# Performance work log

Measured on AMD Instinct MI355X. Metric: run time of the kernel, lower is better.

## Reference

```python
import jax, jax.numpy as jnp
import numpy as np

N, D, H, E_RAW = 100000, 128, 8, 1600000
C = D // H  # head dim = 16
NEG_SLOPE = 0.2
LN_EPS = 1e-5


def _glorot(key, shape):
    fan_in, fan_out = shape[0], shape[-1]
    lim = (6.0 / (fan_in + fan_out)) ** 0.5
    return jax.random.uniform(key, shape, jnp.float32, -lim, lim)


def setup_inputs() -> dict:
    key = jax.random.key(0)
    ks = jax.random.split(key, 16)
    inp = {
        "x": jax.random.normal(ks[0], (N, D), jnp.float32),
        "edge_index": jax.random.randint(ks[1], (2, E_RAW), 0, N, jnp.int64),
    }
    for l in range(2):
        o = 2 + 4 * l
        inp[f"Wl{l}"] = _glorot(ks[o + 0], (D, H * C))
        inp[f"Wr{l}"] = _glorot(ks[o + 1], (D, H * C))
        inp[f"att{l}"] = _glorot(ks[o + 2], (H, C))
        inp[f"b{l}"] = jnp.zeros((H * C,), jnp.float32)
        inp[f"g{l}"] = jnp.ones((D,), jnp.float32)
        inp[f"beta{l}"] = jnp.zeros((D,), jnp.float32)
    return inp


def _gatv2_layer(x, src, dst, Wl, Wr, att, b):
    # GATv2Conv: e_ij = att . leaky_relu(Wl x_j + Wr x_i); softmax over j -> i
    xl = (x @ Wl).reshape(N, H, C)  # source transform
    xr = (x @ Wr).reshape(N, H, C)  # target transform
    m = jax.nn.leaky_relu(xl[src] + xr[dst], NEG_SLOPE)  # [E,H,C]
    e = jnp.einsum("ehc,hc->eh", m, att)  # [E,H]
    emax = jax.ops.segment_max(e, dst, num_segments=N)[dst]
    ex = jnp.exp(e - emax)
    denom = jax.ops.segment_sum(ex, dst, num_segments=N)[dst]
    alpha = ex / denom  # per-destination softmax
    out = jax.ops.segment_sum(xl[src] * alpha[:, :, None], dst, num_segments=N)
    return out.reshape(N, H * C) + b


def _layernorm(x, g, beta):
    mu = jnp.mean(x, axis=-1, keepdims=True)
    var = jnp.var(x, axis=-1, keepdims=True)
    return (x - mu) * jax.lax.rsqrt(var + LN_EPS) * g + beta


def reference(x, edge_index, Wl0, Wr0, att0, b0, g0, beta0,
              Wl1, Wr1, att1, b1, g1, beta1):
    # add_self_loops=True (PyG default): every node attends to itself
    loop = jnp.arange(N, dtype=edge_index.dtype)
    src = jnp.concatenate([edge_index[0], loop])
    dst = jnp.concatenate([edge_index[1], loop])
    params = [(Wl0, Wr0, att0, b0, g0, beta0), (Wl1, Wr1, att1, b1, g1, beta1)]
    for Wl, Wr, att, b, g, beta in params:
        residual = x
        h = _gatv2_layer(x, src, dst, Wl, Wr, att, b)  # dropout is identity (eval)
        h = jax.nn.elu(h)
        x = _layernorm(h + residual, g, beta)
    return x
```

## Files before the change

kernel.cpp:

```cpp
#include <hip/hip_runtime.h>
#include <cstdint>

#define LEAKY 0.2f
#define LN_EPS 1e-5f

typedef __attribute__((ext_vector_type(8))) short short8;
typedef __attribute__((ext_vector_type(4))) float f32x4;
typedef __attribute__((ext_vector_type(2))) float f32x2;

__device__ __forceinline__ ushort bf16_rne(float x) {
    unsigned u = __float_as_uint(x);
    unsigned r = (u + 0x7fffu + ((u >> 16) & 1u)) >> 16;
    return (ushort)r;
}
__device__ __forceinline__ float bf16_to_f(ushort h) {
    return __uint_as_float(((unsigned)h) << 16);
}

__global__ void hist_part(const int* __restrict__ ei, int er, int etot, int n,
                          int* __restrict__ deg) {
    const int xcd = blockIdx.x & 7;
    const int lo = (int)((long long)n * xcd >> 3);
    const int hi = (int)((long long)n * (xcd + 1) >> 3);
    const int stride = (gridDim.x >> 3) * blockDim.x;
    for (int e = (blockIdx.x >> 3) * blockDim.x + threadIdx.x; e < etot;
         e += stride) {
        int dst = (e < er) ? ei[er + e] : (e - er);
        if (dst >= lo && dst < hi) atomicAdd(&deg[dst], 1);
    }
}

__global__ void fill_part(const int* __restrict__ ei, int er, int etot, int n,
                          int* __restrict__ woff, int* __restrict__ colv) {
    const int xcd = blockIdx.x & 7;
    const int lo = (int)((long long)n * xcd >> 3);
    const int hi = (int)((long long)n * (xcd + 1) >> 3);
    const int stride = (gridDim.x >> 3) * blockDim.x;
    for (int e = (blockIdx.x >> 3) * blockDim.x + threadIdx.x; e < etot;
         e += stride) {
        int dst = (e < er) ? ei[er + e] : (e - er);
        if (dst >= lo && dst < hi) {
            int src = (e < er) ? ei[e] : dst;
            int pos = atomicAdd(&woff[dst], 1);
            colv[pos] = src;
        }
    }
}

__global__ __launch_bounds__(1024) void scanA(const int* __restrict__ deg,
                                              int* __restrict__ escan,
                                              int* __restrict__ bsum, int n) {
    __shared__ int wsum[16], wpre[16];
    const int lane = threadIdx.x & 63, wv = threadIdx.x >> 6;
    const int i = blockIdx.x * 1024 + threadIdx.x;
    int v = (i < n) ? deg[i] : 0;
    int x = v;
#pragma unroll
    for (int off = 1; off < 64; off <<= 1) {
        int y = __shfl_up(x, off, 64);
        if (lane >= off) x += y;
    }
    if (lane == 63) wsum[wv] = x;
    __syncthreads();
    if (wv == 0) {
        int s = (lane < 16) ? wsum[lane] : 0;
#pragma unroll
        for (int off = 1; off < 16; off <<= 1) {
            int y = __shfl_up(s, off, 64);
            if (lane >= off) s += y;
        }
        if (lane < 16) wpre[lane] = s;
    }
    __syncthreads();
    int excl = x - v + (wv ? wpre[wv - 1] : 0);
    if (i < n) escan[i] = excl;
    if (threadIdx.x == 1023) bsum[blockIdx.x] = wpre[15];
}

__global__ __launch_bounds__(1024) void scanB(const int* __restrict__ bsum,
                                              int* __restrict__ bpre, int nb,
                                              int* __restrict__ offs, int n) {
    __shared__ int wsum[16], wpre[16];
    const int lane = threadIdx.x & 63, wv = threadIdx.x >> 6;
    const int i = threadIdx.x;
    int v = (i < nb) ? bsum[i] : 0;
    int x = v;
#pragma unroll
    for (int off = 1; off < 64; off <<= 1) {
        int y = __shfl_up(x, off, 64);
        if (lane >= off) x += y;
    }
    if (lane == 63) wsum[wv] = x;
    __syncthreads();
    if (wv == 0) {
        int s = (lane < 16) ? wsum[lane] : 0;
#pragma unroll
        for (int off = 1; off < 16; off <<= 1) {
            int y = __shfl_up(s, off, 64);
            if (lane >= off) s += y;
        }
        if (lane < 16) wpre[lane] = s;
    }
    __syncthreads();
    if (i < nb) bpre[i] = x - v + (wv ? wpre[wv - 1] : 0);
    if (threadIdx.x == 1023) offs[n] = wpre[15];
}

__global__ void scanC(const int* __restrict__ escan, const int* __restrict__ bpre,
                      int* __restrict__ offs, int* __restrict__ woff, int n) {
    int i = blockIdx.x * 256 + threadIdx.x;
    if (i >= n) return;
    int o = escan[i] + bpre[i >> 10];
    offs[i] = o;
    woff[i] = o;
}

__global__ void cvt_w2(const float* __restrict__ Wl0, const float* __restrict__ Wr0,
                       const float* __restrict__ Wl1, const float* __restrict__ Wr1,
                       ushort* __restrict__ Whi, ushort* __restrict__ Wlo) {
    int t = blockIdx.x * 256 + threadIdx.x;
    int layer = t >> 15;
    int i = t & 32767;
    int colblk = i >> 11;
    int ks = (i >> 9) & 3;
    int lane = (i >> 3) & 63;
    int j = i & 7;
    int col = colblk * 16 + (lane & 15);
    int k = ks * 32 + (lane >> 4) * 8 + j;
    const float* Wl = layer ? Wl1 : Wl0;
    const float* Wr = layer ? Wr1 : Wr0;
    float v = (col < 128) ? Wl[(size_t)k * 128 + col]
                          : Wr[(size_t)k * 128 + (col - 128)];
    ushort h = bf16_rne(v);
    Whi[t] = h;
    Wlo[t] = bf16_rne(v - bf16_to_f(h));
}

__global__ __launch_bounds__(256) void gemm_mfma(
    const float* __restrict__ X,
    const ushort* __restrict__ Wfhi, const ushort* __restrict__ Wflo,
    uint* __restrict__ Olb, uint* __restrict__ Orb, int nrows) {
    __shared__ float xs[64 * 32 * 4];
    const int t = threadIdx.x;
    const int wave = t >> 6, lane = t & 63;
    const int m0 = blockIdx.x * 64;
    {
        const float4* Xv = (const float4*)X + (size_t)m0 * 32;
        float4* xsv = (float4*)xs;
#pragma unroll
        for (int i = 0; i < 8; ++i) {
            int idx = i * 256 + t;
            int row = idx >> 5, kc = idx & 31;
            float4 v = {0.f, 0.f, 0.f, 0.f};
            if (m0 + row < nrows) v = Xv[idx];
            xsv[row * 32 + (kc ^ (row & 7))] = v;
        }
    }
    __syncthreads();

    const int lrow = lane & 15;
    const int lkc = (lane >> 4) * 2;
    f32x4 acc[4][4];
#pragma unroll
    for (int mt = 0; mt < 4; ++mt)
#pragma unroll
        for (int nt = 0; nt < 4; ++nt) acc[mt][nt] = (f32x4){0.f, 0.f, 0.f, 0.f};

#pragma unroll 1
    for (int ks = 0; ks < 4; ++ks) {
        short8 ahi[4], alo[4];
#pragma unroll
        for (int mt = 0; mt < 4; ++mt) {
            const int row = mt * 16 + lrow;
            const int kc0 = ks * 8 + lkc;
            float4 v0 = ((const float4*)xs)[row * 32 + (kc0 ^ (row & 7))];
            float4 v1 = ((const float4*)xs)[row * 32 + ((kc0 + 1) ^ (row & 7))];
            float e[8];
            e[0] = v0.x; e[1] = v0.y; e[2] = v0.z; e[3] = v0.w;
            e[4] = v1.x; e[5] = v1.y; e[6] = v1.z; e[7] = v1.w;
#pragma unroll
            for (int j = 0; j < 8; ++j) {
                ushort h = (ushort)(__float_as_uint(e[j]) >> 16);
                ahi[mt][j] = (short)h;
                alo[mt][j] = (short)bf16_rne(e[j] - bf16_to_f(h));
            }
        }
#pragma unroll
        for (int nt = 0; nt < 4; ++nt) {
            size_t off = (((size_t)(wave * 4 + nt) * 4 + ks) * 64 + lane) * 8;
            short8 bhi = *(const short8*)&Wfhi[off];
            short8 blo = *(const short8*)&Wflo[off];
#pragma unroll
            for (int mt = 0; mt < 4; ++mt) {
                acc[mt][nt] = __builtin_amdgcn_mfma_f32_16x16x32_bf16(
                    alo[mt], bhi, acc[mt][nt], 0, 0, 0);
                acc[mt][nt] = __builtin_amdgcn_mfma_f32_16x16x32_bf16(
                    ahi[mt], blo, acc[mt][nt], 0, 0, 0);
                acc[mt][nt] = __builtin_amdgcn_mfma_f32_16x16x32_bf16(
                    ahi[mt], bhi, acc[mt][nt], 0, 0, 0);
            }
        }
    }
    uint* __restrict__ O = (wave < 2) ? Olb : Orb;
    const int cbase = (wave * 64) & 127;
    const int crow0 = (lane >> 4) * 4;
    const bool evn = (lane & 1) == 0;
#pragma unroll
    for (int mt = 0; mt < 4; ++mt) {
#pragma unroll
        for (int i = 0; i < 4; ++i) {
            const int row = m0 + mt * 16 + crow0 + i;
#pragma unroll
            for (int nt = 0; nt < 4; ++nt) {
                float val = acc[mt][nt][i];
                float pv = __shfl_xor(val, 1);
                uint pk = (uint)bf16_rne(val) | ((uint)bf16_rne(pv) << 16);
                if (evn && row < nrows) {
                    const int col = cbase + nt * 16 + lrow;
                    O[(size_t)row * 64 + (col >> 1)] = pk;
                }
            }
        }
    }
}

__global__ __launch_bounds__(256) void gat_agg(
    const uint* __restrict__ xl, const uint* __restrict__ xr,
    const int* __restrict__ offs, const int* __restrict__ colv,
    const float* __restrict__ att,
    const float* __restrict__ bias, const float* __restrict__ gamma,
    const float* __restrict__ beta, const float* __restrict__ resid,
    float* __restrict__ out, int nnode) {
    const int lane = threadIdx.x & 63;
    const int wave0 = blockIdx.x * 4 + (threadIdx.x >> 6);
    const int wstride = gridDim.x * 4;
    const uint* __restrict__ xlb = xl + lane;
    const f32x2 att2 = ((const f32x2*)att)[lane];
    const f32x2 b2 = ((const f32x2*)bias)[lane];
    const f32x2 g2 = ((const f32x2*)gamma)[lane];
    const f32x2 be2 = ((const f32x2*)beta)[lane];
    for (int gid = wave0; gid < nnode; gid += wstride) {
        const uint xru = __builtin_nontemporal_load(xr + (size_t)gid * 64 + lane);
        const float xrx = __uint_as_float(xru << 16);
        const float xry = __uint_as_float(xru & 0xffff0000u);
        float den = 0.f, acc0 = 0.f, acc1 = 0.f;
        int e = offs[gid];
        const int e1 = offs[gid + 1];
        for (; e + 4 <= e1; e += 4) {
            int s0 = colv[e], s1 = colv[e + 1], s2 = colv[e + 2], s3 = colv[e + 3];
            uint u0 = xlb[(size_t)s0 * 64];
            uint u1 = xlb[(size_t)s1 * 64];
            uint u2 = xlb[(size_t)s2 * 64];
            uint u3 = xlb[(size_t)s3 * 64];
            float a0x = __uint_as_float(u0 << 16), a0y = __uint_as_float(u0 & 0xffff0000u);
            float a1x = __uint_as_float(u1 << 16), a1y = __uint_as_float(u1 & 0xffff0000u);
            float a2x = __uint_as_float(u2 << 16), a2y = __uint_as_float(u2 & 0xffff0000u);
            float a3x = __uint_as_float(u3 << 16), a3y = __uint_as_float(u3 & 0xffff0000u);
            float m0x = a0x + xrx, m0y = a0y + xry;
            float m1x = a1x + xrx, m1y = a1y + xry;
            float m2x = a2x + xrx, m2y = a2y + xry;
            float m3x = a3x + xrx, m3y = a3y + xry;
            m0x = fmaxf(m0x, LEAKY * m0x); m0y = fmaxf(m0y, LEAKY * m0y);
            m1x = fmaxf(m1x, LEAKY * m1x); m1y = fmaxf(m1y, LEAKY * m1y);
            m2x = fmaxf(m2x, LEAKY * m2x); m2y = fmaxf(m2y, LEAKY * m2y);
            m3x = fmaxf(m3x, LEAKY * m3x); m3y = fmaxf(m3y, LEAKY * m3y);
            float p0 = m0x * att2.x + m0y * att2.y;
            float p1 = m1x * att2.x + m1y * att2.y;
            float p2 = m2x * att2.x + m2y * att2.y;
            float p3 = m3x * att2.x + m3y * att2.y;
            p0 += __shfl_xor(p0, 1); p0 += __shfl_xor(p0, 2); p0 += __shfl_xor(p0, 4);
            p1 += __shfl_xor(p1, 1); p1 += __shfl_xor(p1, 2); p1 += __shfl_xor(p1, 4);
            p2 += __shfl_xor(p2, 1); p2 += __shfl_xor(p2, 2); p2 += __shfl_xor(p2, 4);
            p3 += __shfl_xor(p3, 1); p3 += __shfl_xor(p3, 2); p3 += __shfl_xor(p3, 4);
            float ex0 = __expf(p0), ex1 = __expf(p1);
            float ex2 = __expf(p2), ex3 = __expf(p3);
            den += (ex0 + ex1) + (ex2 + ex3);
            acc0 += a0x * ex0 + a1x * ex1 + a2x * ex2 + a3x * ex3;
            acc1 += a0y * ex0 + a1y * ex1 + a2y * ex2 + a3y * ex3;
        }
        for (; e < e1; ++e) {
            int s0 = colv[e];
            uint u0 = xlb[(size_t)s0 * 64];
            float a0x = __uint_as_float(u0 << 16), a0y = __uint_as_float(u0 & 0xffff0000u);
            float m0x = a0x + xrx, m0y = a0y + xry;
            m0x = fmaxf(m0x, LEAKY * m0x);
            m0y = fmaxf(m0y, LEAKY * m0y);
            float p0 = m0x * att2.x + m0y * att2.y;
            p0 += __shfl_xor(p0, 1); p0 += __shfl_xor(p0, 2); p0 += __shfl_xor(p0, 4);
            float ex0 = __expf(p0);
            den += ex0;
            acc0 += a0x * ex0;
            acc1 += a0y * ex0;
        }
        float inv_den = 1.f / den;
        float v0 = acc0 * inv_den + b2.x;
        float v1 = acc1 * inv_den + b2.y;
        v0 = v0 > 0.f ? v0 : expm1f(v0);
        v1 = v1 > 0.f ? v1 : expm1f(v1);
        const f32x2 r2 = __builtin_nontemporal_load(
            (const f32x2*)resid + (size_t)gid * 64 + lane);
        float t0 = v0 + r2.x, t1 = v1 + r2.y;
        float s = t0 + t1, ss = t0 * t0 + t1 * t1;
#pragma unroll
        for (int m = 1; m < 64; m <<= 1) {
            s += __shfl_xor(s, m);
            ss += __shfl_xor(ss, m);
        }
        const float mu = s * 0.0078125f;
        const float var = ss * 0.0078125f - mu * mu;
        const float iv = rsqrtf(var + LN_EPS);
        f32x2 o;
        o.x = (t0 - mu) * iv * g2.x + be2.x;
        o.y = (t1 - mu) * iv * g2.y + be2.y;
        __builtin_nontemporal_store(o, (f32x2*)out + (size_t)gid * 64 + lane);
    }
}

extern "C" void kernel_launch(void* const* d_in, const int* in_sizes, int n_in,
                              void* d_out, int out_size, void* d_ws, size_t ws_size,
                              hipStream_t stream) {
    const float* x   = (const float*)d_in[0];
    const int*   ei  = (const int*)d_in[1];
    const float* Wl0 = (const float*)d_in[2];
    const float* Wr0 = (const float*)d_in[3];
    const float* at0 = (const float*)d_in[4];
    const float* b0  = (const float*)d_in[5];
    const float* g0  = (const float*)d_in[6];
    const float* be0 = (const float*)d_in[7];
    const float* Wl1 = (const float*)d_in[8];
    const float* Wr1 = (const float*)d_in[9];
    const float* at1 = (const float*)d_in[10];
    const float* b1  = (const float*)d_in[11];
    const float* g1  = (const float*)d_in[12];
    const float* be1 = (const float*)d_in[13];

    const int NF = in_sizes[0];
    const int n  = NF / 128;
    const int er = in_sizes[1] / 2;
    const int etot = er + n;
    const int nb = (n + 1023) / 1024;

    uint* A     = (uint*)d_ws;
    uint* B     = A + (size_t)NF / 2;
    ushort* Whi = (ushort*)(B + (size_t)NF / 2);
    ushort* Wlo = Whi + 65536;
    int* deg    = (int*)(Wlo + 65536);
    int* woff   = deg + n;
    int* offs   = woff + n;
    int* escan  = offs + (n + 1);
    int* bsum   = escan + n;
    int* bpre   = bsum + 1024;
    int* colv   = bpre + 1024;
    float* C    = (float*)d_out;

    (void)hipMemsetAsync(deg, 0, (size_t)n * sizeof(int), stream);
    hist_part<<<2048, 256, 0, stream>>>(ei, er, etot, n, deg);
    scanA<<<nb, 1024, 0, stream>>>(deg, escan, bsum, n);
    scanB<<<1, 1024, 0, stream>>>(bsum, bpre, nb, offs, n);
    scanC<<<(n + 255) / 256, 256, 0, stream>>>(escan, bpre, offs, woff, n);
    fill_part<<<2048, 256, 0, stream>>>(ei, er, etot, n, woff, colv);
    cvt_w2<<<256, 256, 0, stream>>>(Wl0, Wr0, Wl1, Wr1, Whi, Wlo);

    const int gblk = (n + 63) / 64;

    gemm_mfma<<<gblk, 256, 0, stream>>>(x, Whi, Wlo, A, B, n);
    gat_agg<<<2048, 256, 0, stream>>>(A, B, offs, colv, at0, b0, g0, be0,
                                      x, C, n);
    gemm_mfma<<<gblk, 256, 0, stream>>>(C, Whi + 32768, Wlo + 32768, A, B, n);
    gat_agg<<<2048, 256, 0, stream>>>(A, B, offs, colv, at1, b1, g1, be1,
                                      C, C, n);
}
```

Before: 470.5 us.

## Store layer-1 output as bf16 and skip lo-part MFMA in second GEMM

The first aggregation kernel now writes its layer-norm output as packed bf16 into a new workspace buffer. The second GEMM reads that bf16 input directly and drops the A-low split MFMA pass, and the second aggregation reads the bf16 residual. This halves intermediate traffic for one activation tensor and cuts a third of the MFMAs in the second GEMM. It also makes source indices wave-uniform via readfirstlane. The cost is bf16 rounding of the intermediate activations, including the residual path, which can reduce accuracy.

Result: faster. 445.4 us (-5.4%).

```diff
diff --git a/kernel.cpp b/kernel.cpp
--- a/kernel.cpp
+++ b/kernel.cpp
@@ -15,6 +15,12 @@
 }
 __device__ __forceinline__ float bf16_to_f(ushort h) {
     return __uint_as_float(((unsigned)h) << 16);
+}
+__device__ __forceinline__ f32x2 unpk(uint u) {
+    f32x2 r;
+    r.x = __uint_as_float(u << 16);
+    r.y = __uint_as_float(u & 0xffff0000u);
+    return r;
 }
 
 __global__ void hist_part(const int* __restrict__ ei, int er, int etot, int n,
@@ -136,24 +142,35 @@
     Wlo[t] = bf16_rne(v - bf16_to_f(h));
 }
 
+template <bool ABF16>
 __global__ __launch_bounds__(256) void gemm_mfma(
-    const float* __restrict__ X,
+    const void* __restrict__ Xin,
     const ushort* __restrict__ Wfhi, const ushort* __restrict__ Wflo,
     uint* __restrict__ Olb, uint* __restrict__ Orb, int nrows) {
-    __shared__ float xs[64 * 32 * 4];
+    __shared__ float4 xs[64 * 32];
     const int t = threadIdx.x;
     const int wave = t >> 6, lane = t & 63;
     const int m0 = blockIdx.x * 64;
-    {
-        const float4* Xv = (const float4*)X + (size_t)m0 * 32;
-        float4* xsv = (float4*)xs;
+    if (ABF16) {
+        const uint4* Xv = (const uint4*)Xin + (size_t)m0 * 16;
+        uint4* xsb = (uint4*)xs;
+#pragma unroll
+        for (int i = 0; i < 4; ++i) {
+            int idx = i * 256 + t;
+            int row = idx >> 4, kc = idx & 15;
+            uint4 v = {0u, 0u, 0u, 0u};
+            if (m0 + row < nrows) v = Xv[idx];
+            xsb[row * 16 + (kc ^ (row & 7))] = v;
+        }
+    } else {
+        const float4* Xv = (const float4*)Xin + (size_t)m0 * 32;
 #pragma unroll
         for (int i = 0; i < 8; ++i) {
             int idx = i * 256 + t;
             int row = idx >> 5, kc = idx & 31;
             float4 v = {0.f, 0.f, 0.f, 0.f};
             if (m0 + row < nrows) v = Xv[idx];
-            xsv[row * 32 + (kc ^ (row & 7))] = v;
+            xs[row * 32 + (kc ^ (row & 7))] = v;
         }
     }
     __syncthreads();
@@ -172,17 +189,23 @@
 #pragma unroll
         for (int mt = 0; mt < 4; ++mt) {
             const int row = mt * 16 + lrow;
-            const int kc0 = ks * 8 + lkc;
-            float4 v0 = ((const float4*)xs)[row * 32 + (kc0 ^ (row & 7))];
-            float4 v1 = ((const float4*)xs)[row * 32 + ((kc0 + 1) ^ (row & 7))];
-            float e[8];
-            e[0] = v0.x; e[1] = v0.y; e[2] = v0.z; e[3] = v0.w;
-            e[4] = v1.x; e[5] = v1.y; e[6] = v1.z; e[7] = v1.w;
-#pragma unroll
-            for (int j = 0; j < 8; ++j) {
-                ushort h = (ushort)(__float_as_uint(e[j]) >> 16);
-                ahi[mt][j] = (short)h;
-                alo[mt][j] = (short)bf16_rne(e[j] - bf16_to_f(h));
+            if (ABF16) {
+                const int slot = ks * 4 + (lane >> 4);
+                uint4 w = ((const uint4*)xs)[row * 16 + (slot ^ (row & 7))];
+                ahi[mt] = *(const short8*)&w;
+            } else {
+                const int kc0 = ks * 8 + lkc;
+                float4 v0 = xs[row * 32 + (kc0 ^ (row & 7))];
+                float4 v1 = xs[row * 32 + ((kc0 + 1) ^ (row & 7))];
+                float e[8];
+                e[0] = v0.x; e[1] = v0.y; e[2] = v0.z; e[3] = v0.w;
+                e[4] = v1.x; e[5] = v1.y; e[6] = v1.z; e[7] = v1.w;
+#pragma unroll
+                for (int j = 0; j < 8; ++j) {
+                    ushort h = (ushort)(__float_as_uint(e[j]) >> 16);
+                    ahi[mt][j] = (short)h;
+                    alo[mt][j] = (short)bf16_rne(e[j] - bf16_to_f(h));
+                }
             }
         }
 #pragma unroll
@@ -192,8 +215,9 @@
             short8 blo = *(const short8*)&Wflo[off];
 #pragma unroll
             for (int mt = 0; mt < 4; ++mt) {
-                acc[mt][nt] = __builtin_amdgcn_mfma_f32_16x16x32_bf16(
-                    alo[mt], bhi, acc[mt][nt], 0, 0, 0);
+                if (!ABF16)
+                    acc[mt][nt] = __builtin_amdgcn_mfma_f32_16x16x32_bf16(
+                        alo[mt], bhi, acc[mt][nt], 0, 0, 0);
                 acc[mt][nt] = __builtin_amdgcn_mfma_f32_16x16x32_bf16(
                     ahi[mt], blo, acc[mt][nt], 0, 0, 0);
                 acc[mt][nt] = __builtin_amdgcn_mfma_f32_16x16x32_bf16(
@@ -224,50 +248,48 @@
     }
 }
 
+template <bool RBF16, bool OBF16>
 __global__ __launch_bounds__(256) void gat_agg(
     const uint* __restrict__ xl, const uint* __restrict__ xr,
     const int* __restrict__ offs, const int* __restrict__ colv,
     const float* __restrict__ att,
     const float* __restrict__ bias, const float* __restrict__ gamma,
-    const float* __restrict__ beta, const float* __restrict__ resid,
-    float* __restrict__ out, int nnode) {
+    const float* __restrict__ beta, const void* __restrict__ resid,
+    void* __restrict__ out, int nnode) {
     const int lane = threadIdx.x & 63;
-    const int wave0 = blockIdx.x * 4 + (threadIdx.x >> 6);
+    const int wid = __builtin_amdgcn_readfirstlane(threadIdx.x >> 6);
+    const int wave0 = blockIdx.x * 4 + wid;
     const int wstride = gridDim.x * 4;
-    const uint* __restrict__ xlb = xl + lane;
     const f32x2 att2 = ((const f32x2*)att)[lane];
     const f32x2 b2 = ((const f32x2*)bias)[lane];
     const f32x2 g2 = ((const f32x2*)gamma)[lane];
     const f32x2 be2 = ((const f32x2*)beta)[lane];
     for (int gid = wave0; gid < nnode; gid += wstride) {
         const uint xru = __builtin_nontemporal_load(xr + (size_t)gid * 64 + lane);
-        const float xrx = __uint_as_float(xru << 16);
-        const float xry = __uint_as_float(xru & 0xffff0000u);
-        float den = 0.f, acc0 = 0.f, acc1 = 0.f;
+        const f32x2 xr2 = unpk(xru);
+        float den = 0.f;
+        f32x2 acc = {0.f, 0.f};
         int e = offs[gid];
         const int e1 = offs[gid + 1];
         for (; e + 4 <= e1; e += 4) {
-            int s0 = colv[e], s1 = colv[e + 1], s2 = colv[e + 2], s3 = colv[e + 3];
-            uint u0 = xlb[(size_t)s0 * 64];
-            uint u1 = xlb[(size_t)s1 * 64];
-            uint u2 = xlb[(size_t)s2 * 64];
-            uint u3 = xlb[(size_t)s3 * 64];
-            float a0x = __uint_as_float(u0 << 16), a0y = __uint_as_float(u0 & 0xffff0000u);
-            float a1x = __uint_as_float(u1 << 16), a1y = __uint_as_float(u1 & 0xffff0000u);
-            float a2x = __uint_as_float(u2 << 16), a2y = __uint_as_float(u2 & 0xffff0000u);
-            float a3x = __uint_as_float(u3 << 16), a3y = __uint_as_float(u3 & 0xffff0000u);
-            float m0x = a0x + xrx, m0y = a0y + xry;
-            float m1x = a1x + xrx, m1y = a1y + xry;
-            float m2x = a2x + xrx, m2y = a2y + xry;
-            float m3x = a3x + xrx, m3y = a3y + xry;
-            m0x = fmaxf(m0x, LEAKY * m0x); m0y = fmaxf(m0y, LEAKY * m0y);
-            m1x = fmaxf(m1x, LEAKY * m1x); m1y = fmaxf(m1y, LEAKY * m1y);
-            m2x = fmaxf(m2x, LEAKY * m2x); m2y = fmaxf(m2y, LEAKY * m2y);
-            m3x = fmaxf(m3x, LEAKY * m3x); m3y = fmaxf(m3y, LEAKY * m3y);
-            float p0 = m0x * att2.x + m0y * att2.y;
-            float p1 = m1x * att2.x + m1y * att2.y;
-            float p2 = m2x * att2.x + m2y * att2.y;
-            float p3 = m3x * att2.x + m3y * att2.y;
+            int s0 = __builtin_amdgcn_readfirstlane(colv[e]);
+            int s1 = __builtin_amdgcn_readfirstlane(colv[e + 1]);
+            int s2 = __builtin_amdgcn_readfirstlane(colv[e + 2]);
+            int s3 = __builtin_amdgcn_readfirstlane(colv[e + 3]);
+            uint u0 = xl[(size_t)s0 * 64 + lane];
+            uint u1 = xl[(size_t)s1 * 64 + lane];
+            uint u2 = xl[(size_t)s2 * 64 + lane];
+            uint u3 = xl[(size_t)s3 * 64 + lane];
+            f32x2 a0 = unpk(u0), a1 = unpk(u1), a2 = unpk(u2), a3 = unpk(u3);
+            f32x2 m0 = a0 + xr2, m1 = a1 + xr2, m2 = a2 + xr2, m3 = a3 + xr2;
+            f32x2 l0 = m0 * LEAKY, l1 = m1 * LEAKY, l2 = m2 * LEAKY, l3 = m3 * LEAKY;
+            m0.x = fmaxf(m0.x, l0.x); m0.y = fmaxf(m0.y, l0.y);
+            m1.x = fmaxf(m1.x, l1.x); m1.y = fmaxf(m1.y, l1.y);
+            m2.x = fmaxf(m2.x, l2.x); m2.y = fmaxf(m2.y, l2.y);
+            m3.x = fmaxf(m3.x, l3.x); m3.y = fmaxf(m3.y, l3.y);
+            f32x2 t0 = m0 * att2, t1 = m1 * att2, t2 = m2 * att2, t3 = m3 * att2;
+            float p0 = t0.x + t0.y, p1 = t1.x + t1.y;
+            float p2 = t2.x + t2.y, p3 = t3.x + t3.y;
             p0 += __shfl_xor(p0, 1); p0 += __shfl_xor(p0, 2); p0 += __shfl_xor(p0, 4);
             p1 += __shfl_xor(p1, 1); p1 += __shfl_xor(p1, 2); p1 += __shfl_xor(p1, 4);
             p2 += __shfl_xor(p2, 1); p2 += __shfl_xor(p2, 2); p2 += __shfl_xor(p2, 4);
@@ -275,32 +297,40 @@
             float ex0 = __expf(p0), ex1 = __expf(p1);
             float ex2 = __expf(p2), ex3 = __expf(p3);
             den += (ex0 + ex1) + (ex2 + ex3);
-            acc0 += a0x * ex0 + a1x * ex1 + a2x * ex2 + a3x * ex3;
-            acc1 += a0y * ex0 + a1y * ex1 + a2y * ex2 + a3y * ex3;
+            acc += a0 * ex0;
+            acc += a1 * ex1;
+            acc += a2 * ex2;
+            acc += a3 * ex3;
         }
         for (; e < e1; ++e) {
-            int s0 = colv[e];
-            uint u0 = xlb[(size_t)s0 * 64];
-            float a0x = __uint_as_float(u0 << 16), a0y = __uint_as_float(u0 & 0xffff0000u);
-            float m0x = a0x + xrx, m0y = a0y + xry;
-            m0x = fmaxf(m0x, LEAKY * m0x);
-            m0y = fmaxf(m0y, LEAKY * m0y);
-            float p0 = m0x * att2.x + m0y * att2.y;
+            int s0 = __builtin_amdgcn_readfirstlane(colv[e]);
+            uint u0 = xl[(size_t)s0 * 64 + lane];
+            f32x2 a0 = unpk(u0);
+            f32x2 m0 = a0 + xr2;
+            f32x2 l0 = m0 * LEAKY;
+            m0.x = fmaxf(m0.x, l0.x); m0.y = fmaxf(m0.y, l0.y);
+            f32x2 t0 = m0 * att2;
+            float p0 = t0.x + t0.y;
             p0 += __shfl_xor(p0, 1); p0 += __shfl_xor(p0, 2); p0 += __shfl_xor(p0, 4);
             float ex0 = __expf(p0);
             den += ex0;
-            acc0 += a0x * ex0;
-            acc1 += a0y * ex0;
-        }
-        float inv_den = 1.f / den;
-        float v0 = acc0 * inv_den + b2.x;
-        float v1 = acc1 * inv_den + b2.y;
-        v0 = v0 > 0.f ? v0 : expm1f(v0);
-        v1 = v1 > 0.f ? v1 : expm1f(v1);
-        const f32x2 r2 = __builtin_nontemporal_load(
-            (const f32x2*)resid + (size_t)gid * 64 + lane);
-        float t0 = v0 + r2.x, t1 = v1 + r2.y;
-        float s = t0 + t1, ss = t0 * t0 + t1 * t1;
+            acc += a0 * ex0;
+        }
+        const float inv_den = 1.f / den;
+        f32x2 v = acc * inv_den + b2;
+        v.x = v.x > 0.f ? v.x : expm1f(v.x);
+        v.y = v.y > 0.f ? v.y : expm1f(v.y);
+        f32x2 r2;
+        if (RBF16) {
+            uint ru = __builtin_nontemporal_load(
+                (const uint*)resid + (size_t)gid * 64 + lane);
+            r2 = unpk(ru);
+        } else {
+            r2 = __builtin_nontemporal_load(
+                (const f32x2*)resid + (size_t)gid * 64 + lane);
+        }
+        f32x2 tv = v + r2;
+        float s = tv.x + tv.y, ss = tv.x * tv.x + tv.y * tv.y;
 #pragma unroll
         for (int m = 1; m < 64; m <<= 1) {
             s += __shfl_xor(s, m);
@@ -309,10 +339,13 @@
         const float mu = s * 0.0078125f;
         const float var = ss * 0.0078125f - mu * mu;
         const float iv = rsqrtf(var + LN_EPS);
-        f32x2 o;
-        o.x = (t0 - mu) * iv * g2.x + be2.x;
-        o.y = (t1 - mu) * iv * g2.y + be2.y;
-        __builtin_nontemporal_store(o, (f32x2*)out + (size_t)gid * 64 + lane);
+        f32x2 o = (tv - mu) * iv * g2 + be2;
+        if (OBF16) {
+            uint po = (uint)bf16_rne(o.x) | ((uint)bf16_rne(o.y) << 16);
+            __builtin_nontemporal_store(po, (uint*)out + (size_t)gid * 64 + lane);
+        } else {
+            __builtin_nontemporal_store(o, (f32x2*)out + (size_t)gid * 64 + lane);
+        }
     }
 }
 
@@ -342,12 +375,13 @@
 
     uint* A     = (uint*)d_ws;
     uint* B     = A + (size_t)NF / 2;
-    ushort* Whi = (ushort*)(B + (size_t)NF / 2);
+    uint* C1    = B + (size_t)NF / 2;
+    ushort* Whi = (ushort*)(C1 + (size_t)NF / 2);
     ushort* Wlo = Whi + 65536;
     int* deg    = (int*)(Wlo + 65536);
     int* woff   = deg + n;
     int* offs   = woff + n;
-    int* escan  = offs + (n + 1);
+    int* escan  = offs + (n + 4);
     int* bsum   = escan + n;
     int* bpre   = bsum + 1024;
     int* colv   = bpre + 1024;
@@ -363,10 +397,11 @@
 
     const int gblk = (n + 63) / 64;
 
-    gemm_mfma<<<gblk, 256, 0, stream>>>(x, Whi, Wlo, A, B, n);
-    gat_agg<<<2048, 256, 0, stream>>>(A, B, offs, colv, at0, b0, g0, be0,
-                                      x, C, n);
-    gemm_mfma<<<gblk, 256, 0, stream>>>(C, Whi + 32768, Wlo + 32768, A, B, n);
-    gat_agg<<<2048, 256, 0, stream>>>(A, B, offs, colv, at1, b1, g1, be1,
-                                      C, C, n);
-}
+    gemm_mfma<false><<<gblk, 256, 0, stream>>>(x, Whi, Wlo, A, B, n);
+    gat_agg<false, true><<<2048, 256, 0, stream>>>(
+        A, B, offs, colv, at0, b0, g0, be0, x, C1, n);
+    gemm_mfma<true><<<gblk, 256, 0, stream>>>(C1, Whi + 32768, Wlo + 32768,
+                                              A, B, n);
+    gat_agg<true, false><<<2048, 256, 0, stream>>>(
+        A, B, offs, colv, at1, b1, g1, be1, C1, C, n);
+}
```
